# Kernel tuning notes

Measured on AMD Instinct MI355X. Metric: run time of the kernel, lower is better.

Reference implementation:

```python
import jax, jax.numpy as jnp
import numpy as np

T, B, E = 1024, 4, 1024
H = 16
D = E // H          # head_dim = 64
L = 16              # max_relative_length


def setup_inputs() -> dict:
    key = jax.random.key(0)
    ks = jax.random.split(key, 4)
    query = jax.random.normal(ks[0], (T, B, E), dtype=jnp.float32)
    # xavier-ish scaled params
    in_proj_weight = jax.random.normal(ks[1], (3 * E, E), dtype=jnp.float32) * (1.0 / np.sqrt(E))
    in_proj_bias = jnp.zeros((3 * E,), dtype=jnp.float32)
    rel_pos_keys = jax.random.normal(ks[2], (2 * L + 1, E), dtype=jnp.float32) * (1.0 / np.sqrt(E))
    out_w = jax.random.normal(ks[3], (E, E), dtype=jnp.float32) * (1.0 / np.sqrt(E))
    out_b = jnp.zeros((E,), dtype=jnp.float32)
    return {"query": query, "in_proj_weight": in_proj_weight, "in_proj_bias": in_proj_bias,
            "rel_pos_keys": rel_pos_keys, "out_w": out_w, "out_b": out_b}


def reference(query, in_proj_weight, in_proj_bias, rel_pos_keys, out_w, out_b):
    t, b, e = query.shape
    scaling = D ** (-0.5)
    # fused qkv projection: [T,B,3E]
    qkv = jnp.einsum('tbe,fe->tbf', query, in_proj_weight) + in_proj_bias
    q, k, v = jnp.split(qkv, 3, axis=-1)
    q = q * scaling
    # [T,B,E] -> [B*H, T, D]
    def heads(x):
        return x.reshape(t, b * H, D).transpose(1, 0, 2)
    q, k, v = heads(q), heads(k), heads(v)
    # clipped relative position matrix [T,T] in [0, 2L]
    r = jnp.arange(t)
    dist = jnp.clip(r[None, :] - r[:, None], -L, L) + L
    # gather relation keys, keep first head_dim channels: [T,T,D]
    rel_k = rel_pos_keys[dist][:, :, :D]
    # scores = q k^T + q . rel_k  (Shaw et al.), [B*H, T, T]
    scores = jnp.einsum('btd,bsd->bts', q, k) + jnp.einsum('btd,tsd->bts', q, rel_k)
    probs = jax.nn.softmax(scores, axis=-1)
    attn = jnp.einsum('bts,bsd->btd', probs, v)      # [B*H, T, D]
    attn = attn.transpose(1, 0, 2).reshape(t, b, e)   # [T, B, E]
    return jnp.einsum('tbe,oe->tbo', attn, out_w) + out_b
```

## Files before the change

### kernel.cpp

```cpp
#include <hip/hip_runtime.h>
#include <hip/hip_bf16.h>

typedef __attribute__((ext_vector_type(8))) short short8;
typedef __attribute__((ext_vector_type(4))) float floatx4;


#define QSCALE 0.18033688011112043f

__device__ __forceinline__ short f2bf(float x) {
  union { float f; unsigned u; } cv; cv.f = x;
  unsigned u = cv.u + (0x7FFFu + ((cv.u >> 16) & 1u));
  return (short)(u >> 16);
}

__device__ __forceinline__ unsigned pk_bf16(float a, float b) {
  union { __hip_bfloat162 h; unsigned u; } cv;
  cv.h = __float22bfloat162_rn(make_float2(a, b));
  return cv.u;
}

__device__ __forceinline__ float exp2_hw(float x) {
  return __builtin_amdgcn_exp2f(x);
}

__device__ __forceinline__ floatx4 mfma16(short8 a, short8 b, floatx4 c) {
  return __builtin_amdgcn_mfma_f32_16x16x32_bf16(a, b, c, 0, 0, 0);
}

__device__ __forceinline__ void async_copy16(const void* g, void* l) {
  __builtin_amdgcn_global_load_lds((const __attribute__((address_space(1))) void*)g,
                                   (__attribute__((address_space(3))) void*)l, 16, 0, 0);
}

__global__ void __launch_bounds__(256) convert_all_kernel(
    const float* __restrict__ s0, const float* __restrict__ s1,
    const float* __restrict__ s2,
    short* __restrict__ d0, short* __restrict__ d1, short* __restrict__ d2)
{
  int i = blockIdx.x * 256 + threadIdx.x;
  if (i < 524288) {
    int e8 = i & 127, b = (i >> 7) & 3, t = i >> 9;
    const float4* s = (const float4*)s0 + (size_t)i * 2;
    float4 a = s[0], c = s[1];
    uint4 o = make_uint4(pk_bf16(a.x, a.y), pk_bf16(a.z, a.w),
                         pk_bf16(c.x, c.y), pk_bf16(c.z, c.w));
    *(uint4*)(d0 + (size_t)b * 1048576 + t * 1024 + e8 * 8) = o;
  } else {
    const float* src; short* dst; int off;
    if (i < 917504) { src = s1; dst = d1; off = i - 524288; }
    else            { src = s2; dst = d2; off = i - 917504; }
    const float4* s = (const float4*)src + (size_t)off * 2;
    float4 a = s[0], c = s[1];
    uint4 o = make_uint4(pk_bf16(a.x, a.y), pk_bf16(a.z, a.w),
                         pk_bf16(c.x, c.y), pk_bf16(c.z, c.w));
    *(uint4*)(dst + (size_t)off * 8) = o;
  }
}

__global__ void __launch_bounds__(512, 2) gemm_qkv(
    const short* __restrict__ A, const short* __restrict__ W,
    const float* __restrict__ bias,
    short* __restrict__ q_ws, short* __restrict__ k_ws, short* __restrict__ v_ws)
{
  __shared__ __align__(16) short Atile[2 * 256 * 64];
  __shared__ __align__(16) short Btile[2 * 192 * 64];
  const int tid = threadIdx.x, lane = tid & 63, w = tid >> 6;
  const int quad = lane >> 4, l16 = lane & 15;
  const int m0 = blockIdx.x * 256, n0 = blockIdx.y * 192;
  const int wmh = (w >> 2);
  const int wn = (w & 3) * 48;

  const short* Ag = A + (size_t)m0 * 1024;
  const short* Wg = W + (size_t)n0 * 1024;

  floatx4 acc[8][3];
  #pragma unroll
  for (int mt = 0; mt < 8; mt++)
    #pragma unroll
    for (int nt = 0; nt < 3; nt++) acc[mt][nt] = (floatx4)(0.0f);

  #define STAGE_A(kc, buf)                                                   \
    {                                                                        \
      _Pragma("unroll")                                                      \
      for (int i = 0; i < 4; i++) {                                          \
        int seg = i * 512 + tid;                                             \
        int row = seg >> 3, p = seg & 7;                                     \
        int ck = p ^ (row & 7);                                              \
        async_copy16(Ag + (size_t)row * 1024 + (kc) * 64 + ck * 8,           \
                     Atile + (buf) * 16384 + (size_t)(i * 512 + w * 64) * 8);\
      }                                                                      \
    }
  #define STAGE_B(kc, buf)                                                   \
    {                                                                        \
      _Pragma("unroll")                                                      \
      for (int i = 0; i < 3; i++) {                                          \
        int seg = i * 512 + tid;                                             \
        int row = seg >> 3, p = seg & 7;                                     \
        int ck = p ^ (row & 7);                                              \
        async_copy16(Wg + (size_t)row * 1024 + (kc) * 64 + ck * 8,           \
                     Btile + (buf) * 12288 + (size_t)(i * 512 + w * 64) * 8);\
      }                                                                      \
    }

  STAGE_A(0, 0); STAGE_B(0, 0);
  asm volatile("s_waitcnt vmcnt(0)" ::: "memory");
  __builtin_amdgcn_s_barrier();

  for (int kt = 0; kt < 16; ++kt) {
    const int cur = kt & 1, nxt = cur ^ 1;
    const int kc1 = (kt + 1 < 16) ? kt + 1 : 15;

    STAGE_A(kc1, nxt); STAGE_B(kc1, nxt);

    short8 af[8][2], bf[3][2];
    #pragma unroll
    for (int mt = 0; mt < 8; mt++) {
      int r = mt * 16 + l16;
      int gr = wmh * 128 + r;
      #pragma unroll
      for (int ks = 0; ks < 2; ks++)
        af[mt][ks] = *(const short8*)(Atile + cur * 16384 + gr * 64
                                      + (((quad + 4 * ks) ^ (r & 7)) << 3));
    }
    #pragma unroll
    for (int nt = 0; nt < 3; nt++) {
      int row = wn + nt * 16 + l16;
      #pragma unroll
      for (int ks = 0; ks < 2; ks++)
        bf[nt][ks] = *(const short8*)(Btile + cur * 12288 + row * 64
                                      + (((quad + 4 * ks) ^ (row & 7)) << 3));
    }

    __builtin_amdgcn_s_setprio(1);
    #pragma unroll
    for (int mt = 0; mt < 8; mt++)
      #pragma unroll
      for (int nt = 0; nt < 3; nt++)
        #pragma unroll
        for (int ks = 0; ks < 2; ks++)
          acc[mt][nt] = mfma16(af[mt][ks], bf[nt][ks], acc[mt][nt]);
    __builtin_amdgcn_s_setprio(0);
    __builtin_amdgcn_sched_barrier(0);

    asm volatile("s_waitcnt vmcnt(0)" ::: "memory");
    __builtin_amdgcn_s_barrier();
  }
  #undef STAGE_A
  #undef STAGE_B

  #pragma unroll
  for (int nt = 0; nt < 3; nt++) {
    int f = n0 + wn + nt * 16 + l16;
    float bv = bias[f];
    int which = f >> 10;
    int h = (f >> 6) & 15;
    int d = f & 63;
    if (which == 2) {
      #pragma unroll
      for (int mt = 0; mt < 8; mt++) {
        int r0 = m0 + wmh * 128 + mt * 16 + quad * 4;
        int t = r0 & 1023, bb = r0 >> 10;
        int bh = bb * 16 + h;
        unsigned lo = pk_bf16(acc[mt][nt][0] + bv, acc[mt][nt][1] + bv);
        unsigned hi = pk_bf16(acc[mt][nt][2] + bv, acc[mt][nt][3] + bv);
        *(uint2*)(v_ws + ((size_t)bh * 64 + d) * 1024 + t) = make_uint2(lo, hi);
      }
    } else {
      short* dst = which ? k_ws : q_ws;
      const float sc = which ? 1.0f : QSCALE;
      #pragma unroll
      for (int mt = 0; mt < 8; mt++) {
        int r0 = m0 + wmh * 128 + mt * 16 + quad * 4;
        int t = r0 & 1023, bb = r0 >> 10;
        int bh = bb * 16 + h;
        unsigned u01 = pk_bf16((acc[mt][nt][0] + bv) * sc, (acc[mt][nt][1] + bv) * sc);
        unsigned u23 = pk_bf16((acc[mt][nt][2] + bv) * sc, (acc[mt][nt][3] + bv) * sc);
        size_t base = ((size_t)bh * 1024 + t) * 64 + d;
        dst[base]           = (short)u01;
        dst[base + 64]      = (short)(u01 >> 16);
        dst[base + 128]     = (short)u23;
        dst[base + 192]     = (short)(u23 >> 16);
      }
    }
  }
}

__global__ void __launch_bounds__(512, 4) attn_kernel(
    const short* __restrict__ q_ws, const short* __restrict__ k_ws,
    const short* __restrict__ v_ws, const float* __restrict__ relk,
    short* __restrict__ attn_ws)
{
  __shared__ float rel_lds[128 * 33];
  __shared__ __align__(16) short Ktile[2][64 * 64];
  __shared__ __align__(16) short Vtile[2][64 * 64];
  __shared__ __align__(16) short p_lds[8][16 * 64];
  const int tid = threadIdx.x, lane = tid & 63, w = tid >> 6;
  const int quad = lane >> 4, l16 = lane & 15;
  const int bh = 8 * ((int)blockIdx.x & 7) + (((int)blockIdx.x >> 3) & 7);
  const int t0 = ((int)blockIdx.x >> 6) * 128;
  const int b = bh >> 4, h = bh & 15;

  short8 aq[2];
  #pragma unroll
  for (int ks = 0; ks < 2; ks++)
    aq[ks] = *(const short8*)(q_ws
        + ((size_t)bh * 1024 + t0 + w * 16 + l16) * 64 + ks * 32 + quad * 8);

  if (tid < 384) {
    int row = tid >> 3, p = tid & 7;
    short8 val;
    if (row < 33) {
      const float* src = relk + row * 1024 + p * 8;
      float4 a = *(const float4*)src, c = *(const float4*)(src + 4);
      val[0] = f2bf(a.x); val[1] = f2bf(a.y); val[2] = f2bf(a.z); val[3] = f2bf(a.w);
      val[4] = f2bf(c.x); val[5] = f2bf(c.y); val[6] = f2bf(c.z); val[7] = f2bf(c.w);
    } else {
      val = (short8)0;
    }
    *(short8*)(Ktile[0] + row * 64 + ((p ^ (row & 7)) << 3)) = val;
  }
  __syncthreads();

  #pragma unroll
  for (int jt = 0; jt < 3; jt++) {
    floatx4 scR = (floatx4)(0.0f);
    #pragma unroll
    for (int ks = 0; ks < 2; ks++) {
      int rrow = jt * 16 + l16;
      int ck = (quad + 4 * ks) ^ (rrow & 7);
      short8 rb = *(const short8*)(Ktile[0] + rrow * 64 + ck * 8);
      scR = mfma16(aq[ks], rb, scR);
    }
    int j = jt * 16 + l16;
    if (j < 33) {
      #pragma unroll
      for (int reg = 0; reg < 4; reg++) {
        int tl = w * 16 + quad * 4 + reg;
        rel_lds[tl * 33 + j] = scR[reg];
      }
    }
  }
  __syncthreads();

  const float biasLo = rel_lds[(w * 16 + l16) * 33 + 0];
  const float biasHi = rel_lds[(w * 16 + l16) * 33 + 32];

  floatx4 o[4];
  #pragma unroll
  for (int dt = 0; dt < 4; dt++) o[dt] = (floatx4)(0.0f);
  floatx4 rsacc = (floatx4)(0.0f);
  short8 vone;
  #pragma unroll
  for (int i = 0; i < 8; i++) vone[i] = (short)0x3F80;

  const short* kg = k_ws + (size_t)bh * 1024 * 64;
  const short* vg = v_ws + (size_t)bh * 64 * 1024;

  #define STAGE_KV(S0, BUF)                                                  \
    {                                                                        \
      int row = tid >> 3, p = tid & 7;                                       \
      int ck = p ^ (row & 7);                                                \
      async_copy16(kg + (size_t)((S0) + row) * 64 + ck * 8,                  \
                   Ktile[BUF] + (size_t)w * 512);                            \
      async_copy16(vg + (size_t)row * 1024 + (S0) + ck * 8,                  \
                   Vtile[BUF] + (size_t)w * 512);                            \
    }

  STAGE_KV(0, 0);

  for (int st = 0; st < 16; st++) {
    const int s0 = st * 64;
    const int cur = st & 1;
    __syncthreads();
    if (st < 15) STAGE_KV(s0 + 64, 1 - cur);

    const int qbase = t0 + w * 16;
    const bool alllo = (s0 <= qbase - 79);
    const bool allhi = (s0 >= qbase + 31);
    const bool diag = !(alllo || allhi);
    const float initv = alllo ? biasLo : (allhi ? biasHi : 0.0f);

    #pragma unroll
    for (int nt = 0; nt < 4; nt++) {
      short8 kb0, kb1;
      {
        int srow = nt * 16 + l16;
        kb0 = *(const short8*)(Ktile[cur] + srow * 64
                               + ((quad ^ (l16 & 7)) << 3));
        kb1 = *(const short8*)(Ktile[cur] + srow * 64
                               + ((((quad + 4)) ^ (l16 & 7)) << 3));
      }
      floatx4 sc = (floatx4)(initv);
      __builtin_amdgcn_s_setprio(1);
      sc = mfma16(kb0, aq[0], sc);
      sc = mfma16(kb1, aq[1], sc);
      __builtin_amdgcn_s_setprio(0);
      if (diag) {
        int ql = w * 16 + l16;
        #pragma unroll
        for (int reg = 0; reg < 4; reg++) {
          int delta = (s0 + 16 * nt + 4 * quad + reg) - (qbase + l16);
          delta = min(max(delta, -16), 16) + 16;
          sc[reg] += rel_lds[ql * 33 + delta];
        }
      }
      #pragma unroll
      for (int reg = 0; reg < 4; reg++) sc[reg] = exp2_hw(sc[reg]);
      unsigned w0 = pk_bf16(sc[0], sc[1]);
      unsigned w1 = pk_bf16(sc[2], sc[3]);
      int srot = (16 * nt + 4 * quad + 4 * l16) & 63;
      *(uint2*)(p_lds[w] + l16 * 64 + srot) = make_uint2(w0, w1);
    }

    short8 ap[2];
    #pragma unroll
    for (int ks = 0; ks < 2; ks++) {
      int s1 = (32 * ks + 8 * quad + 4 * l16) & 63;
      int s2 = (s1 + 4) & 63;
      union { short8 v; uint2 u[2]; } pu;
      pu.u[0] = *(const uint2*)(p_lds[w] + l16 * 64 + s1);
      pu.u[1] = *(const uint2*)(p_lds[w] + l16 * 64 + s2);
      ap[ks] = pu.v;
    }

    __builtin_amdgcn_s_setprio(1);
    rsacc = mfma16(ap[0], vone, rsacc);
    rsacc = mfma16(ap[1], vone, rsacc);
    #pragma unroll
    for (int dt = 0; dt < 4; dt++) {
      short8 vb0, vb1;
      {
        int drow = dt * 16 + l16;
        vb0 = *(const short8*)(Vtile[cur] + drow * 64
                               + ((quad ^ (l16 & 7)) << 3));
        vb1 = *(const short8*)(Vtile[cur] + drow * 64
                               + (((quad + 4) ^ (l16 & 7)) << 3));
      }
      o[dt] = mfma16(ap[0], vb0, o[dt]);
      o[dt] = mfma16(ap[1], vb1, o[dt]);
    }
    __builtin_amdgcn_s_setprio(0);
  }
  #undef STAGE_KV

  float inv_[4];
  #pragma unroll
  for (int reg = 0; reg < 4; reg++) inv_[reg] = 1.0f / rsacc[reg];
  #pragma unroll
  for (int dt = 0; dt < 4; dt++) {
    unsigned u01 = pk_bf16(o[dt][0] * inv_[0], o[dt][1] * inv_[1]);
    unsigned u23 = pk_bf16(o[dt][2] * inv_[2], o[dt][3] * inv_[3]);
    int tg = t0 + w * 16 + quad * 4;
    size_t base = ((size_t)tg * 4 + b) * 1024 + h * 64 + dt * 16 + l16;
    attn_ws[base]         = (short)u01;
    attn_ws[base + 4096]  = (short)(u01 >> 16);
    attn_ws[base + 8192]  = (short)u23;
    attn_ws[base + 12288] = (short)(u23 >> 16);
  }
}

__global__ void __launch_bounds__(512, 2) gemm_outproj(
    const short* __restrict__ A, const short* __restrict__ W,
    const float* __restrict__ bias, float* __restrict__ out)
{
  __shared__ __align__(16) short Atile[2 * 128 * 64];
  __shared__ __align__(16) short Btile[2 * 128 * 64];
  const int tid = threadIdx.x, lane = tid & 63, w = tid >> 6;
  const int quad = lane >> 4, l16 = lane & 15;
  const int m0 = blockIdx.x * 128, n0 = blockIdx.y * 128;
  const int wmh = (w >> 2);
  const int wn = (w & 3) * 32;

  const short* Ag = A + (size_t)m0 * 1024;
  const short* Wg = W + (size_t)n0 * 1024;

  floatx4 acc[4][2];
  #pragma unroll
  for (int mt = 0; mt < 4; mt++)
    #pragma unroll
    for (int nt = 0; nt < 2; nt++) acc[mt][nt] = (floatx4)(0.0f);

  #define STAGE_OP(kc, buf)                                                  \
    {                                                                        \
      _Pragma("unroll")                                                      \
      for (int i = 0; i < 2; i++) {                                          \
        int seg = i * 512 + tid;                                             \
        int row = seg >> 3, p = seg & 7;                                     \
        int ck = p ^ (row & 7);                                              \
        async_copy16(Ag + (size_t)row * 1024 + (kc) * 64 + ck * 8,           \
                     Atile + (buf) * 8192 + (size_t)(i * 512 + w * 64) * 8); \
        async_copy16(Wg + (size_t)row * 1024 + (kc) * 64 + ck * 8,           \
                     Btile + (buf) * 8192 + (size_t)(i * 512 + w * 64) * 8); \
      }                                                                      \
    }

  STAGE_OP(0, 0);
  asm volatile("s_waitcnt vmcnt(0)" ::: "memory");
  __builtin_amdgcn_s_barrier();

  for (int kt = 0; kt < 16; ++kt) {
    const int cur = kt & 1, nxt = cur ^ 1;
    const int kc1 = (kt + 1 < 16) ? kt + 1 : 15;

    STAGE_OP(kc1, nxt);

    short8 af[4][2], bf[2][2];
    #pragma unroll
    for (int mt = 0; mt < 4; mt++) {
      int gr = wmh * 64 + mt * 16 + l16;
      #pragma unroll
      for (int ks = 0; ks < 2; ks++)
        af[mt][ks] = *(const short8*)(Atile + cur * 8192 + gr * 64
                                      + (((quad + 4 * ks) ^ (gr & 7)) << 3));
    }
    #pragma unroll
    for (int nt = 0; nt < 2; nt++) {
      int row = wn + nt * 16 + l16;
      #pragma unroll
      for (int ks = 0; ks < 2; ks++)
        bf[nt][ks] = *(const short8*)(Btile + cur * 8192 + row * 64
                                      + (((quad + 4 * ks) ^ (row & 7)) << 3));
    }

    __builtin_amdgcn_s_setprio(1);
    #pragma unroll
    for (int mt = 0; mt < 4; mt++)
      #pragma unroll
      for (int nt = 0; nt < 2; nt++)
        #pragma unroll
        for (int ks = 0; ks < 2; ks++)
          acc[mt][nt] = mfma16(af[mt][ks], bf[nt][ks], acc[mt][nt]);
    __builtin_amdgcn_s_setprio(0);
    __builtin_amdgcn_sched_barrier(0);

    asm volatile("s_waitcnt vmcnt(0)" ::: "memory");
    __builtin_amdgcn_s_barrier();
  }
  #undef STAGE_OP

  #pragma unroll
  for (int nt = 0; nt < 2; nt++) {
    int f = n0 + wn + nt * 16 + l16;
    float bv = bias[f];
    #pragma unroll
    for (int mt = 0; mt < 4; mt++) {
      #pragma unroll
      for (int reg = 0; reg < 4; reg++) {
        int r = m0 + wmh * 64 + mt * 16 + quad * 4 + reg;
        out[(size_t)r * 1024 + f] = acc[mt][nt][reg] + bv;
      }
    }
  }
}

extern "C" void kernel_launch(void* const* d_in, const int* in_sizes, int n_in,
                              void* d_out, int out_size, void* d_ws, size_t ws_size,
                              hipStream_t stream) {
  const float* query = (const float*)d_in[0];
  const float* in_w  = (const float*)d_in[1];
  const float* in_b  = (const float*)d_in[2];
  const float* relk  = (const float*)d_in[3];
  const float* out_w = (const float*)d_in[4];
  const float* out_b = (const float*)d_in[5];
  float* out = (float*)d_out;

  short* qry_bf = (short*)d_ws;
  short* win_bf = qry_bf + (size_t)4096 * 1024;
  short* wout_bf = win_bf + (size_t)3072 * 1024;
  short* q_ws   = wout_bf + (size_t)1024 * 1024;
  short* k_ws   = q_ws + (size_t)64 * 1024 * 64;
  short* v_ws   = k_ws + (size_t)64 * 1024 * 64;
  short* att_ws = v_ws + (size_t)64 * 1024 * 64;

  convert_all_kernel<<<4096, 256, 0, stream>>>(query, in_w, out_w,
                                               qry_bf, win_bf, wout_bf);
  gemm_qkv<<<dim3(16, 16), 512, 0, stream>>>(qry_bf, win_bf, in_b, q_ws, k_ws, v_ws);
  attn_kernel<<<512, 512, 0, stream>>>(q_ws, k_ws, v_ws, relk, att_ws);
  gemm_outproj<<<dim3(32, 8), 512, 0, stream>>>(att_ws, wout_bf, out_b, out);
}
```

Baseline: 164.3 us.

## Process two query tiles per wave in attention to reuse K/V tiles

Each attention block now covers 256 query rows instead of 128: every wave holds two 16-row query fragments and reuses each loaded K and V LDS fragment for both. The grid is halved to 256 blocks, and the LDS buffers for relative scores and P are doubled. The aim is to halve K/V global traffic and LDS fragment reads per unit of compute, at the cost of more registers per wave, a lower occupancy target, and fewer blocks to spread across the CUs.

After: 167.3 us. About the same (+1.8%).

```diff
diff --git a/kernel.cpp b/kernel.cpp
--- a/kernel.cpp
+++ b/kernel.cpp
@@ -185,26 +185,29 @@
   }
 }
 
-__global__ void __launch_bounds__(512, 4) attn_kernel(
+__global__ void __launch_bounds__(512, 2) attn_kernel(
     const short* __restrict__ q_ws, const short* __restrict__ k_ws,
     const short* __restrict__ v_ws, const float* __restrict__ relk,
     short* __restrict__ attn_ws)
 {
-  __shared__ float rel_lds[128 * 33];
+  __shared__ float rel_lds[256 * 33];
   __shared__ __align__(16) short Ktile[2][64 * 64];
   __shared__ __align__(16) short Vtile[2][64 * 64];
-  __shared__ __align__(16) short p_lds[8][16 * 64];
+  __shared__ __align__(16) short p_lds[16][16 * 64];
   const int tid = threadIdx.x, lane = tid & 63, w = tid >> 6;
   const int quad = lane >> 4, l16 = lane & 15;
   const int bh = 8 * ((int)blockIdx.x & 7) + (((int)blockIdx.x >> 3) & 7);
-  const int t0 = ((int)blockIdx.x >> 6) * 128;
+  const int t0 = ((int)blockIdx.x >> 6) * 256;
   const int b = bh >> 4, h = bh & 15;
 
-  short8 aq[2];
-  #pragma unroll
-  for (int ks = 0; ks < 2; ks++)
-    aq[ks] = *(const short8*)(q_ws
-        + ((size_t)bh * 1024 + t0 + w * 16 + l16) * 64 + ks * 32 + quad * 8);
+  short8 aq[2][2];
+  #pragma unroll
+  for (int qt = 0; qt < 2; qt++)
+    #pragma unroll
+    for (int ks = 0; ks < 2; ks++)
+      aq[qt][ks] = *(const short8*)(q_ws
+          + ((size_t)bh * 1024 + t0 + qt * 128 + w * 16 + l16) * 64
+          + ks * 32 + quad * 8);
 
   if (tid < 384) {
     int row = tid >> 3, p = tid & 7;
@@ -222,33 +225,44 @@
   __syncthreads();
 
   #pragma unroll
-  for (int jt = 0; jt < 3; jt++) {
-    floatx4 scR = (floatx4)(0.0f);
-    #pragma unroll
-    for (int ks = 0; ks < 2; ks++) {
-      int rrow = jt * 16 + l16;
-      int ck = (quad + 4 * ks) ^ (rrow & 7);
-      short8 rb = *(const short8*)(Ktile[0] + rrow * 64 + ck * 8);
-      scR = mfma16(aq[ks], rb, scR);
-    }
-    int j = jt * 16 + l16;
-    if (j < 33) {
-      #pragma unroll
-      for (int reg = 0; reg < 4; reg++) {
-        int tl = w * 16 + quad * 4 + reg;
-        rel_lds[tl * 33 + j] = scR[reg];
+  for (int qt = 0; qt < 2; qt++) {
+    #pragma unroll
+    for (int jt = 0; jt < 3; jt++) {
+      floatx4 scR = (floatx4)(0.0f);
+      #pragma unroll
+      for (int ks = 0; ks < 2; ks++) {
+        int rrow = jt * 16 + l16;
+        int ck = (quad + 4 * ks) ^ (rrow & 7);
+        short8 rb = *(const short8*)(Ktile[0] + rrow * 64 + ck * 8);
+        scR = mfma16(aq[qt][ks], rb, scR);
+      }
+      int j = jt * 16 + l16;
+      if (j < 33) {
+        #pragma unroll
+        for (int reg = 0; reg < 4; reg++) {
+          int tl = qt * 128 + w * 16 + quad * 4 + reg;
+          rel_lds[tl * 33 + j] = scR[reg];
+        }
       }
     }
   }
   __syncthreads();
 
-  const float biasLo = rel_lds[(w * 16 + l16) * 33 + 0];
-  const float biasHi = rel_lds[(w * 16 + l16) * 33 + 32];
-
-  floatx4 o[4];
-  #pragma unroll
-  for (int dt = 0; dt < 4; dt++) o[dt] = (floatx4)(0.0f);
-  floatx4 rsacc = (floatx4)(0.0f);
+  float biasLo[2], biasHi[2];
+  #pragma unroll
+  for (int qt = 0; qt < 2; qt++) {
+    int ql = qt * 128 + w * 16 + l16;
+    biasLo[qt] = rel_lds[ql * 33 + 0];
+    biasHi[qt] = rel_lds[ql * 33 + 32];
+  }
+
+  floatx4 o[2][4];
+  #pragma unroll
+  for (int qt = 0; qt < 2; qt++)
+    #pragma unroll
+    for (int dt = 0; dt < 4; dt++) o[qt][dt] = (floatx4)(0.0f);
+  floatx4 rsacc[2];
+  rsacc[0] = (floatx4)(0.0f); rsacc[1] = (floatx4)(0.0f);
   short8 vone;
   #pragma unroll
   for (int i = 0; i < 8; i++) vone[i] = (short)0x3F80;
@@ -274,11 +288,15 @@
     __syncthreads();
     if (st < 15) STAGE_KV(s0 + 64, 1 - cur);
 
-    const int qbase = t0 + w * 16;
-    const bool alllo = (s0 <= qbase - 79);
-    const bool allhi = (s0 >= qbase + 31);
-    const bool diag = !(alllo || allhi);
-    const float initv = alllo ? biasLo : (allhi ? biasHi : 0.0f);
+    bool diag[2]; float initv[2];
+    #pragma unroll
+    for (int qt = 0; qt < 2; qt++) {
+      const int qbase = t0 + qt * 128 + w * 16;
+      bool alllo = (s0 <= qbase - 79);
+      bool allhi = (s0 >= qbase + 31);
+      diag[qt] = !(alllo || allhi);
+      initv[qt] = alllo ? biasLo[qt] : (allhi ? biasHi[qt] : 0.0f);
+    }
 
     #pragma unroll
     for (int nt = 0; nt < 4; nt++) {
@@ -288,44 +306,53 @@
         kb0 = *(const short8*)(Ktile[cur] + srow * 64
                                + ((quad ^ (l16 & 7)) << 3));
         kb1 = *(const short8*)(Ktile[cur] + srow * 64
-                               + ((((quad + 4)) ^ (l16 & 7)) << 3));
-      }
-      floatx4 sc = (floatx4)(initv);
-      __builtin_amdgcn_s_setprio(1);
-      sc = mfma16(kb0, aq[0], sc);
-      sc = mfma16(kb1, aq[1], sc);
-      __builtin_amdgcn_s_setprio(0);
-      if (diag) {
-        int ql = w * 16 + l16;
+                               + (((quad + 4) ^ (l16 & 7)) << 3));
+      }
+      #pragma unroll
+      for (int qt = 0; qt < 2; qt++) {
+        floatx4 sc = (floatx4)(initv[qt]);
+        __builtin_amdgcn_s_setprio(1);
+        sc = mfma16(kb0, aq[qt][0], sc);
+        sc = mfma16(kb1, aq[qt][1], sc);
+        __builtin_amdgcn_s_setprio(0);
+        if (diag[qt]) {
+          int ql = qt * 128 + w * 16 + l16;
+          const int qbase = t0 + qt * 128 + w * 16;
+          #pragma unroll
+          for (int reg = 0; reg < 4; reg++) {
+            int delta = (s0 + 16 * nt + 4 * quad + reg) - (qbase + l16);
+            delta = min(max(delta, -16), 16) + 16;
+            sc[reg] += rel_lds[ql * 33 + delta];
+          }
+        }
         #pragma unroll
-        for (int reg = 0; reg < 4; reg++) {
-          int delta = (s0 + 16 * nt + 4 * quad + reg) - (qbase + l16);
-          delta = min(max(delta, -16), 16) + 16;
-          sc[reg] += rel_lds[ql * 33 + delta];
-        }
-      }
-      #pragma unroll
-      for (int reg = 0; reg < 4; reg++) sc[reg] = exp2_hw(sc[reg]);
-      unsigned w0 = pk_bf16(sc[0], sc[1]);
-      unsigned w1 = pk_bf16(sc[2], sc[3]);
-      int srot = (16 * nt + 4 * quad + 4 * l16) & 63;
-      *(uint2*)(p_lds[w] + l16 * 64 + srot) = make_uint2(w0, w1);
-    }
-
-    short8 ap[2];
-    #pragma unroll
-    for (int ks = 0; ks < 2; ks++) {
-      int s1 = (32 * ks + 8 * quad + 4 * l16) & 63;
-      int s2 = (s1 + 4) & 63;
-      union { short8 v; uint2 u[2]; } pu;
-      pu.u[0] = *(const uint2*)(p_lds[w] + l16 * 64 + s1);
-      pu.u[1] = *(const uint2*)(p_lds[w] + l16 * 64 + s2);
-      ap[ks] = pu.v;
-    }
+        for (int reg = 0; reg < 4; reg++) sc[reg] = exp2_hw(sc[reg]);
+        unsigned w0 = pk_bf16(sc[0], sc[1]);
+        unsigned w1 = pk_bf16(sc[2], sc[3]);
+        int srot = (16 * nt + 4 * quad + 4 * l16) & 63;
+        *(uint2*)(p_lds[w * 2 + qt] + l16 * 64 + srot) = make_uint2(w0, w1);
+      }
+    }
+
+    short8 ap[2][2];
+    #pragma unroll
+    for (int qt = 0; qt < 2; qt++)
+      #pragma unroll
+      for (int ks = 0; ks < 2; ks++) {
+        int s1 = (32 * ks + 8 * quad + 4 * l16) & 63;
+        int s2 = (s1 + 4) & 63;
+        union { short8 v; uint2 u[2]; } pu;
+        pu.u[0] = *(const uint2*)(p_lds[w * 2 + qt] + l16 * 64 + s1);
+        pu.u[1] = *(const uint2*)(p_lds[w * 2 + qt] + l16 * 64 + s2);
+        ap[qt][ks] = pu.v;
+      }
 
     __builtin_amdgcn_s_setprio(1);
-    rsacc = mfma16(ap[0], vone, rsacc);
-    rsacc = mfma16(ap[1], vone, rsacc);
+    #pragma unroll
+    for (int qt = 0; qt < 2; qt++) {
+      rsacc[qt] = mfma16(ap[qt][0], vone, rsacc[qt]);
+      rsacc[qt] = mfma16(ap[qt][1], vone, rsacc[qt]);
+    }
     #pragma unroll
     for (int dt = 0; dt < 4; dt++) {
       short8 vb0, vb1;
@@ -336,26 +363,32 @@
         vb1 = *(const short8*)(Vtile[cur] + drow * 64
                                + (((quad + 4) ^ (l16 & 7)) << 3));
       }
-      o[dt] = mfma16(ap[0], vb0, o[dt]);
-      o[dt] = mfma16(ap[1], vb1, o[dt]);
+      #pragma unroll
+      for (int qt = 0; qt < 2; qt++) {
+        o[qt][dt] = mfma16(ap[qt][0], vb0, o[qt][dt]);
+        o[qt][dt] = mfma16(ap[qt][1], vb1, o[qt][dt]);
+      }
     }
     __builtin_amdgcn_s_setprio(0);
   }
   #undef STAGE_KV
 
-  float inv_[4];
-  #pragma unroll
-  for (int reg = 0; reg < 4; reg++) inv_[reg] = 1.0f / rsacc[reg];
-  #pragma unroll
-  for (int dt = 0; dt < 4; dt++) {
-    unsigned u01 = pk_bf16(o[dt][0] * inv_[0], o[dt][1] * inv_[1]);
-    unsigned u23 = pk_bf16(o[dt][2] * inv_[2], o[dt][3] * inv_[3]);
-    int tg = t0 + w * 16 + quad * 4;
-    size_t base = ((size_t)tg * 4 + b) * 1024 + h * 64 + dt * 16 + l16;
-    attn_ws[base]         = (short)u01;
-    attn_ws[base + 4096]  = (short)(u01 >> 16);
-    attn_ws[base + 8192]  = (short)u23;
-    attn_ws[base + 12288] = (short)(u23 >> 16);
+  #pragma unroll
+  for (int qt = 0; qt < 2; qt++) {
+    float inv_[4];
+    #pragma unroll
+    for (int reg = 0; reg < 4; reg++) inv_[reg] = 1.0f / rsacc[qt][reg];
+    #pragma unroll
+    for (int dt = 0; dt < 4; dt++) {
+      unsigned u01 = pk_bf16(o[qt][dt][0] * inv_[0], o[qt][dt][1] * inv_[1]);
+      unsigned u23 = pk_bf16(o[qt][dt][2] * inv_[2], o[qt][dt][3] * inv_[3]);
+      int tg = t0 + qt * 128 + w * 16 + quad * 4;
+      size_t base = ((size_t)tg * 4 + b) * 1024 + h * 64 + dt * 16 + l16;
+      attn_ws[base]         = (short)u01;
+      attn_ws[base + 4096]  = (short)(u01 >> 16);
+      attn_ws[base + 8192]  = (short)u23;
+      attn_ws[base + 12288] = (short)(u23 >> 16);
+    }
   }
 }
 
@@ -475,6 +508,6 @@
   convert_all_kernel<<<4096, 256, 0, stream>>>(query, in_w, out_w,
                                                qry_bf, win_bf, wout_bf);
   gemm_qkv<<<dim3(16, 16), 512, 0, stream>>>(qry_bf, win_bf, in_b, q_ws, k_ws, v_ws);
-  attn_kernel<<<512, 512, 0, stream>>>(q_ws, k_ws, v_ws, relk, att_ws);
+  attn_kernel<<<256, 512, 0, stream>>>(q_ws, k_ws, v_ws, relk, att_ws);
   gemm_outproj<<<dim3(32, 8), 512, 0, stream>>>(att_ws, wout_bf, out_b, out);
 }
```
